# Kernel tuning notes

Measured on AMD Instinct MI355X. Metric: run time of the kernel, lower is better.

## Reference

```python
import jax, jax.numpy as jnp
import numpy as np

ALPHA = 0.2  # LeakyReLU negative slope
NEG_INF = -9e15


def setup_inputs() -> dict:
    key = jax.random.key(0)
    k1, k2, k3, k4 = jax.random.split(key, 4)
    B, N, D = 8, 2048, 256
    h = jax.random.normal(k1, (B, N, D), dtype=jnp.float32)
    adj = jax.random.randint(k2, (B, N, N), 0, 2, dtype=jnp.int32)
    W = jax.random.normal(k3, (D, D), dtype=jnp.float32) * (1.0 / np.sqrt(D))
    a = jax.random.normal(k4, (2 * D, 1), dtype=jnp.float32) * 0.05
    return {"h": h, "adj": adj, "W": W, "a": a}


def reference(h, adj, W, a):
    # Wh = Linear(h): torch nn.Linear with weight W [out,in] -> h @ W.T
    Wh = jnp.einsum('bnd,od->bno', h, W)            # [B,N,D]
    D = Wh.shape[-1]
    a1, a2 = a[:D, 0], a[D:, 0]                     # split concat-attention vector
    # e_ij = leakyrelu(a1.Wh_i + a2.Wh_j) without materializing [B,N,N,2D]
    s1 = Wh @ a1                                    # [B,N]
    s2 = Wh @ a2                                    # [B,N]
    e = jax.nn.leaky_relu(s1[:, :, None] + s2[:, None, :], negative_slope=ALPHA)
    e = jnp.where(adj > 0, e, NEG_INF)
    attention = jax.nn.softmax(e, axis=-1)          # dropout is identity in eval
    h_prime = jnp.einsum('bij,bjd->bid', attention, Wh)
    return h_prime
```

## Files before the change

kernel.cpp:

```cpp
#include <hip/hip_runtime.h>
#include <cstdint>
#include <cstddef>


#define NB 8
#define NN 2048
#define ND 256
#define ALPHA_F 0.2f
#define JC 64
#define NCH2 32
#define IR 64

typedef __attribute__((ext_vector_type(8))) short short8;
typedef __attribute__((ext_vector_type(4))) float f32x4;
typedef __attribute__((ext_vector_type(4))) int   i32x4;

__device__ __forceinline__ unsigned short f2bf(float f) {
  union { float f; unsigned int u; } v; v.f = f;
  unsigned int r = v.u + 0x7FFFu + ((v.u >> 16) & 1u);
  return (unsigned short)(r >> 16);
}

__device__ __forceinline__ short8 pack8(const float* v) {
  short8 r;
#pragma unroll
  for (int e = 0; e < 8; ++e) r[e] = (short)f2bf(v[e]);
  return r;
}

__device__ __forceinline__ unsigned int cvtpk(float lo, float hi) {
  unsigned int r;
  asm("v_cvt_pk_bf16_f32 %0, %1, %2" : "=v"(r) : "v"(lo), "v"(hi));
  return r;
}

__global__ __launch_bounds__(256) void k_wh(
    const float* __restrict__ h, const float* __restrict__ W,
    const float* __restrict__ a,
    unsigned short* __restrict__ WhT, float* __restrict__ s1g,
    float* __restrict__ s2g)
{
  __shared__ float sl1[64], sl2[64];
  const int tid  = threadIdx.x;
  const int wid  = tid >> 6;
  const int lane = tid & 63;
  const int l15  = lane & 15;
  const int c    = lane >> 4;
  const int r0   = blockIdx.x * 64;
  const int b    = r0 >> 11;
  const int n0   = r0 & 2047;

  if (tid < 64) { sl1[tid] = 0.f; sl2[tid] = 0.f; }

  f32x4 acc[4][4] = {};

  const float* hb = h + (size_t)r0 * ND;
  const int ocol0 = wid * 64;

  for (int k0 = 0; k0 < ND; k0 += 32) {
    short8 afr[4], bfr[4];
#pragma unroll
    for (int mi = 0; mi < 4; ++mi) {
      const float* p = hb + (size_t)(mi * 16 + l15) * ND + k0 + c * 8;
      float t[8];
      *(f32x4*)t       = *(const f32x4*)p;
      *(f32x4*)(t + 4) = *(const f32x4*)(p + 4);
      afr[mi] = pack8(t);
    }
#pragma unroll
    for (int ni = 0; ni < 4; ++ni) {
      const int o = ocol0 + ni * 16 + l15;
      const float* p = W + (size_t)o * ND + k0 + c * 8;
      float t[8];
      *(f32x4*)t       = *(const f32x4*)p;
      *(f32x4*)(t + 4) = *(const f32x4*)(p + 4);
      bfr[ni] = pack8(t);
    }
#pragma unroll
    for (int mi = 0; mi < 4; ++mi)
#pragma unroll
      for (int ni = 0; ni < 4; ++ni)
        acc[mi][ni] = __builtin_amdgcn_mfma_f32_16x16x32_bf16(
            afr[mi], bfr[ni], acc[mi][ni], 0, 0, 0);
  }

  float a1v[4], a2v[4];
#pragma unroll
  for (int ni = 0; ni < 4; ++ni) {
    const int o = ocol0 + ni * 16 + l15;
    a1v[ni] = a[o];
    a2v[ni] = a[ND + o];
  }
  float p1[4][4] = {}, p2[4][4] = {};
#pragma unroll
  for (int mi = 0; mi < 4; ++mi)
#pragma unroll
    for (int ni = 0; ni < 4; ++ni)
#pragma unroll
      for (int r = 0; r < 4; ++r) {
        p1[mi][r] += acc[mi][ni][r] * a1v[ni];
        p2[mi][r] += acc[mi][ni][r] * a2v[ni];
      }
#pragma unroll
  for (int m = 1; m <= 8; m <<= 1) {
#pragma unroll
    for (int mi = 0; mi < 4; ++mi)
#pragma unroll
      for (int r = 0; r < 4; ++r) {
        p1[mi][r] += __shfl_xor(p1[mi][r], m, 64);
        p2[mi][r] += __shfl_xor(p2[mi][r], m, 64);
      }
  }
  __syncthreads();
  if (l15 == 0) {
#pragma unroll
    for (int mi = 0; mi < 4; ++mi)
#pragma unroll
      for (int r = 0; r < 4; ++r) {
        atomicAdd(&sl1[mi * 16 + c * 4 + r], p1[mi][r]);
        atomicAdd(&sl2[mi * 16 + c * 4 + r], p2[mi][r]);
      }
  }

#pragma unroll
  for (int mi = 0; mi < 4; ++mi)
#pragma unroll
    for (int ni = 0; ni < 4; ++ni) {
      const int o = ocol0 + ni * 16 + l15;
      const int n = n0 + mi * 16 + c * 4;
      unsigned short u4[4];
#pragma unroll
      for (int r = 0; r < 4; ++r) u4[r] = f2bf(acc[mi][ni][r]);
      *(uint2*)(WhT + ((size_t)b * ND + o) * NN + n) = *(uint2*)u4;
    }
  __syncthreads();
  if (tid < 64) { s1g[r0 + tid] = sl1[tid]; s2g[r0 + tid] = sl2[tid]; }
}

__global__ __launch_bounds__(512, 2) void k_attn(
    const int* __restrict__ adj, const unsigned short* __restrict__ WhT,
    const float* __restrict__ s1g, const float* __restrict__ s2g,
    float* __restrict__ out)
{
  __shared__ __align__(16) float s2s[NN];
  __shared__ __align__(16) unsigned short pbuf[2][IR * JC];
  __shared__ float lsml[IR];

  const int tid  = threadIdx.x;
  const int wid  = tid >> 6;
  const int lane = tid & 63;
  const int l15  = lane & 15;
  const int c    = lane >> 4;
  const int bid  = blockIdx.x;
  const int b    = bid & 7;
  const int i0   = (bid >> 3) * IR;

  const int row  = tid >> 3;
  const int jseg = tid & 7;
  const int gsw  = jseg ^ (row & 7);

  if (tid < IR) lsml[tid] = 0.f;
  {
    const f32x4* src = (const f32x4*)(s2g + (size_t)b * NN);
    f32x4* dst = (f32x4*)s2s;
    for (int t = tid; t < NN / 4; t += 512) dst[t] = src[t];
  }
  const float s1r = s1g[(size_t)b * NN + i0 + row];
  const int* abt = adj + ((size_t)(b * NN + i0 + row)) * NN + jseg * 8;

  f32x4 acc[4][2] = {};
  float lacc = 0.f;

  const unsigned short* wb = WhT + ((size_t)b * ND + wid * 32) * NN;

  i32x4 adm[4][2];
  short8 bfr[2][2][2];

#define LOADADJ(CH, P)                                                       \
  { const int* ap = abt + (CH) * JC;                                         \
    adm[P][0] = *(const i32x4*)ap;                                           \
    adm[P][1] = *(const i32x4*)(ap + 4); }

#define LOADB(CH, SL)                                                        \
  {                                                                          \
    _Pragma("unroll")                                                        \
    for (int ks = 0; ks < 2; ++ks)                                           \
      _Pragma("unroll")                                                      \
      for (int ni = 0; ni < 2; ++ni)                                         \
        bfr[SL][ks][ni] = *(const short8*)(wb + (size_t)(ni * 16 + l15) * NN + \
                                           (CH) * JC + ks * 32 + c * 8);     \
  }

#define BUILDC(CH, BB, P)                                                    \
  {                                                                          \
    const float* s2p = s2s + (CH) * JC + jseg * 8;                           \
    f32x4 sa = *(const f32x4*)s2p;                                           \
    f32x4 sb = *(const f32x4*)(s2p + 4);                                     \
    float pv[8];                                                             \
    _Pragma("unroll")                                                        \
    for (int e = 0; e < 4; ++e) {                                            \
      float ev = s1r + sa[e];                                                \
      ev = fmaxf(ev, ALPHA_F * ev);                                          \
      pv[e] = (adm[P][0][e] > 0) ? __expf(ev) : 0.f;                         \
    }                                                                        \
    _Pragma("unroll")                                                        \
    for (int e = 0; e < 4; ++e) {                                            \
      float ev = s1r + sb[e];                                                \
      ev = fmaxf(ev, ALPHA_F * ev);                                          \
      pv[4 + e] = (adm[P][1][e] > 0) ? __expf(ev) : 0.f;                     \
    }                                                                        \
    lacc += ((pv[0] + pv[1]) + (pv[2] + pv[3])) +                            \
            ((pv[4] + pv[5]) + (pv[6] + pv[7]));                             \
    i32x4 pk;                                                                \
    pk[0] = (int)cvtpk(pv[0], pv[1]);                                        \
    pk[1] = (int)cvtpk(pv[2], pv[3]);                                        \
    pk[2] = (int)cvtpk(pv[4], pv[5]);                                        \
    pk[3] = (int)cvtpk(pv[6], pv[7]);                                        \
    *(i32x4*)(&pbuf[BB][0] + row * JC + gsw * 8) = pk;                       \
  }

#define CHUNK_BARRIER()                                                      \
  { asm volatile("s_waitcnt lgkmcnt(0)" ::: "memory");                       \
    __builtin_amdgcn_s_barrier(); }

  LOADADJ(0, 0)
  LOADADJ(1, 1)
  LOADADJ(2, 2)
  LOADADJ(3, 3)
  __syncthreads();

  BUILDC(0, 0, 0)
  LOADADJ(4, 0)
  LOADB(0, 0)
  CHUNK_BARRIER()

#pragma unroll
  for (int ch = 0; ch < NCH2; ++ch) {
    const int bb = ch & 1;
    const unsigned short* pbR = &pbuf[bb][0];
    if (ch + 1 < NCH2) LOADB(ch + 1, (ch + 1) & 1)
    if (ch + 1 < NCH2) {
      BUILDC(ch + 1, (ch + 1) & 1, (ch + 1) & 3)
      if (ch + 5 < NCH2) LOADADJ(ch + 5, (ch + 5) & 3)
    }
#pragma unroll
    for (int ks = 0; ks < 2; ++ks) {
#pragma unroll
      for (int mi = 0; mi < 4; ++mi) {
        short8 am = *(const short8*)(pbR + (mi * 16 + l15) * JC +
                                     (((ks * 4 + c) ^ (l15 & 7)) * 8));
#pragma unroll
        for (int ni = 0; ni < 2; ++ni)
          acc[mi][ni] = __builtin_amdgcn_mfma_f32_16x16x32_bf16(
              am, bfr[bb][ks][ni], acc[mi][ni], 0, 0, 0);
      }
    }
    CHUNK_BARRIER()
  }

  lacc += __shfl_xor(lacc, 1, 64);
  lacc += __shfl_xor(lacc, 2, 64);
  lacc += __shfl_xor(lacc, 4, 64);
  if ((lane & 7) == 0) atomicAdd(&lsml[row], lacc);
  __syncthreads();

  float* ob = out + ((size_t)b * NN + i0) * ND + wid * 32;
#pragma unroll
  for (int mi = 0; mi < 4; ++mi)
#pragma unroll
    for (int r = 0; r < 4; ++r) {
      const int rr = mi * 16 + c * 4 + r;
      const float linv = 1.0f / lsml[rr];
#pragma unroll
      for (int ni = 0; ni < 2; ++ni)
        ob[(size_t)rr * ND + ni * 16 + l15] = acc[mi][ni][r] * linv;
    }
#undef BUILDC
#undef LOADB
#undef LOADADJ
#undef CHUNK_BARRIER
}

extern "C" void kernel_launch(void* const* d_in, const int* in_sizes, int n_in,
                              void* d_out, int out_size, void* d_ws, size_t ws_size,
                              hipStream_t stream) {
  const float* h   = (const float*)d_in[0];
  const int*   adj = (const int*)d_in[1];
  const float* W   = (const float*)d_in[2];
  const float* a   = (const float*)d_in[3];
  float* out = (float*)d_out;

  unsigned short* WhT = (unsigned short*)d_ws;
  float* s1g = (float*)((char*)d_ws + (size_t)NB * ND * NN * 2);
  float* s2g = s1g + (size_t)NB * NN;

  k_wh<<<dim3(NB * NN / 64), dim3(256), 0, stream>>>(h, W, a, WhT, s1g, s2g);
  k_attn<<<dim3(NB * NN / IR), dim3(512), 0, stream>>>(adj, WhT, s1g, s2g, out);
}
```

Before: 65.59 us.

## Split attention j-range across two blocks and combine partials in a divide kernel

The attention kernel now splits the key dimension into two halves, launching 512 blocks instead of 256. Each block writes an unnormalized partial output and a partial row sum. A new small kernel adds the two partials and divides by the combined sum. This targets the low block count relative to the CU count, and the launch bound is raised to allow more resident blocks. The cost is an extra launch plus extra global traffic for the partial output (8x2048x256 floats) and its read-back.

```diff
diff --git a/kernel.cpp b/kernel.cpp
--- a/kernel.cpp
+++ b/kernel.cpp
@@ -8,7 +8,7 @@
 #define ND 256
 #define ALPHA_F 0.2f
 #define JC 64
-#define NCH2 32
+#define NCH 16
 #define IR 64
 
 typedef __attribute__((ext_vector_type(8))) short short8;
@@ -137,14 +137,14 @@
   if (tid < 64) { s1g[r0 + tid] = sl1[tid]; s2g[r0 + tid] = sl2[tid]; }
 }
 
-__global__ __launch_bounds__(512, 2) void k_attn(
+__global__ __launch_bounds__(512, 4) void k_attn(
     const int* __restrict__ adj, const unsigned short* __restrict__ WhT,
     const float* __restrict__ s1g, const float* __restrict__ s2g,
-    float* __restrict__ out)
+    float* __restrict__ l0, float* __restrict__ l1,
+    float* __restrict__ part1, float* __restrict__ out)
 {
-  __shared__ __align__(16) float s2s[NN];
+  __shared__ __align__(16) float s2s[NN / 2];
   __shared__ __align__(16) unsigned short pbuf[2][IR * JC];
-  __shared__ float lsml[IR];
 
   const int tid  = threadIdx.x;
   const int wid  = tid >> 6;
@@ -153,27 +153,29 @@
   const int c    = lane >> 4;
   const int bid  = blockIdx.x;
   const int b    = bid & 7;
-  const int i0   = (bid >> 3) * IR;
+  const int rb   = (bid >> 3) & 31;
+  const int jg   = bid >> 8;
+  const int i0   = rb * IR;
+  const int jgbase = jg * (NN / 2);
 
   const int row  = tid >> 3;
   const int jseg = tid & 7;
   const int gsw  = jseg ^ (row & 7);
 
-  if (tid < IR) lsml[tid] = 0.f;
   {
-    const f32x4* src = (const f32x4*)(s2g + (size_t)b * NN);
+    const f32x4* src = (const f32x4*)(s2g + (size_t)b * NN + jgbase);
     f32x4* dst = (f32x4*)s2s;
-    for (int t = tid; t < NN / 4; t += 512) dst[t] = src[t];
+    if (tid < NN / 2 / 4) dst[tid] = src[tid];
   }
   const float s1r = s1g[(size_t)b * NN + i0 + row];
-  const int* abt = adj + ((size_t)(b * NN + i0 + row)) * NN + jseg * 8;
+  const int* abt = adj + ((size_t)(b * NN + i0 + row)) * NN + jgbase + jseg * 8;
 
   f32x4 acc[4][2] = {};
   float lacc = 0.f;
 
-  const unsigned short* wb = WhT + ((size_t)b * ND + wid * 32) * NN;
-
-  i32x4 adm[4][2];
+  const unsigned short* wb = WhT + ((size_t)b * ND + wid * 32) * NN + jgbase;
+
+  i32x4 adm[2][2];
   short8 bfr[2][2][2];
 
 #define LOADADJ(CH, P)                                                       \
@@ -225,23 +227,21 @@
 
   LOADADJ(0, 0)
   LOADADJ(1, 1)
-  LOADADJ(2, 2)
-  LOADADJ(3, 3)
   __syncthreads();
 
   BUILDC(0, 0, 0)
-  LOADADJ(4, 0)
+  LOADADJ(2, 0)
   LOADB(0, 0)
   CHUNK_BARRIER()
 
 #pragma unroll
-  for (int ch = 0; ch < NCH2; ++ch) {
+  for (int ch = 0; ch < NCH; ++ch) {
     const int bb = ch & 1;
     const unsigned short* pbR = &pbuf[bb][0];
-    if (ch + 1 < NCH2) LOADB(ch + 1, (ch + 1) & 1)
-    if (ch + 1 < NCH2) {
-      BUILDC(ch + 1, (ch + 1) & 1, (ch + 1) & 3)
-      if (ch + 5 < NCH2) LOADADJ(ch + 5, (ch + 5) & 3)
+    if (ch + 1 < NCH) LOADB(ch + 1, (ch + 1) & 1)
+    if (ch + 1 < NCH) {
+      BUILDC(ch + 1, (ch + 1) & 1, (ch + 1) & 1)
+      if (ch + 3 < NCH) LOADADJ(ch + 3, (ch + 3) & 1)
     }
 #pragma unroll
     for (int ks = 0; ks < 2; ++ks) {
@@ -261,24 +261,42 @@
   lacc += __shfl_xor(lacc, 1, 64);
   lacc += __shfl_xor(lacc, 2, 64);
   lacc += __shfl_xor(lacc, 4, 64);
-  if ((lane & 7) == 0) atomicAdd(&lsml[row], lacc);
-  __syncthreads();
-
-  float* ob = out + ((size_t)b * NN + i0) * ND + wid * 32;
+  float* lp = (jg ? l1 : l0) + (size_t)b * NN + i0;
+  if ((lane & 7) == 0) lp[row] = lacc;
+
+  float* ob = (jg ? part1 : out) + ((size_t)b * NN + i0) * ND + wid * 32;
 #pragma unroll
   for (int mi = 0; mi < 4; ++mi)
 #pragma unroll
     for (int r = 0; r < 4; ++r) {
       const int rr = mi * 16 + c * 4 + r;
-      const float linv = 1.0f / lsml[rr];
 #pragma unroll
       for (int ni = 0; ni < 2; ++ni)
-        ob[(size_t)rr * ND + ni * 16 + l15] = acc[mi][ni][r] * linv;
+        ob[(size_t)rr * ND + ni * 16 + l15] = acc[mi][ni][r];
     }
 #undef BUILDC
 #undef LOADB
 #undef LOADADJ
 #undef CHUNK_BARRIER
+}
+
+__global__ __launch_bounds__(256) void k_div(
+    float* __restrict__ out, const float* __restrict__ part1,
+    const float* __restrict__ l0, const float* __restrict__ l1)
+{
+  const int t  = threadIdx.x;
+  const int rr = blockIdx.x * 4 + (t >> 6);
+  const float linv = 1.0f / (l0[rr] + l1[rr]);
+  const int idx = t & 63;
+  f32x4* o = (f32x4*)(out + (size_t)rr * ND) + idx;
+  const f32x4* p = (const f32x4*)(part1 + (size_t)rr * ND) + idx;
+  f32x4 v = *o;
+  f32x4 w = *p;
+  v[0] = (v[0] + w[0]) * linv;
+  v[1] = (v[1] + w[1]) * linv;
+  v[2] = (v[2] + w[2]) * linv;
+  v[3] = (v[3] + w[3]) * linv;
+  *o = v;
 }
 
 extern "C" void kernel_launch(void* const* d_in, const int* in_sizes, int n_in,
@@ -290,10 +308,15 @@
   const float* a   = (const float*)d_in[3];
   float* out = (float*)d_out;
 
-  unsigned short* WhT = (unsigned short*)d_ws;
-  float* s1g = (float*)((char*)d_ws + (size_t)NB * ND * NN * 2);
-  float* s2g = s1g + (size_t)NB * NN;
+  char* ws = (char*)d_ws;
+  unsigned short* WhT = (unsigned short*)ws;
+  float* s1g   = (float*)(ws + (size_t)NB * ND * NN * 2);
+  float* s2g   = s1g + (size_t)NB * NN;
+  float* l0    = s2g + (size_t)NB * NN;
+  float* l1    = l0 + (size_t)NB * NN;
+  float* part1 = l1 + (size_t)NB * NN;
 
   k_wh<<<dim3(NB * NN / 64), dim3(256), 0, stream>>>(h, W, a, WhT, s1g, s2g);
-  k_attn<<<dim3(NB * NN / IR), dim3(512), 0, stream>>>(adj, WhT, s1g, s2g, out);
-}
+  k_attn<<<dim3(512), dim3(512), 0, stream>>>(adj, WhT, s1g, s2g, l0, l1, part1, out);
+  k_div<<<dim3(NB * NN / 4), dim3(256), 0, stream>>>(out, part1, l0, l1);
+}
```

Result: slower. 75.37 us (+14.9%).
